# Kernel tuning notes

Measured on AMD Instinct MI355X. Metric: run time of the kernel, lower is better.

The kernel has to match this reference:

```python
import jax, jax.numpy as jnp
import numpy as np

L = 2048         # new tokens (prefill)
HID = 4096
NH = 32          # attention heads
NKV = 8          # kv heads
HD = HID // NH   # 128
MAX = 4096       # kv-cache capacity
EPS = 1e-5


def _rope_tables(L, HD):
    inv_freq = 1.0 / (10000.0 ** (np.arange(0, HD, 2, dtype=np.float32) / HD))
    ang = np.arange(L, dtype=np.float32)[:, None] * inv_freq[None, :]  # [L, HD/2]
    ang = np.concatenate([ang, ang], axis=-1)                          # HF duplicated layout
    return jnp.asarray(np.cos(ang)), jnp.asarray(np.sin(ang))


def setup_inputs() -> dict:
    key = jax.random.key(0)
    ks = jax.random.split(key, 6)
    cos, sin = _rope_tables(L, HD)
    s = 0.02
    return {
        "x": jax.random.normal(ks[0], (L, HID), jnp.float32),
        "cos": cos,
        "sin": sin,
        "position_ids": jnp.arange(L, dtype=jnp.int64),
        "seq_len": L,
        "k_cache": jnp.zeros((MAX, NKV, HD), jnp.float32),
        "v_cache": jnp.zeros((MAX, NKV, HD), jnp.float32),
        "ln_w": jnp.ones((HID,), jnp.float32),
        "Wq": jax.random.normal(ks[1], (NH * HD, HID), jnp.float32) * s,
        "Wk": jax.random.normal(ks[2], (NKV * HD, HID), jnp.float32) * s,
        "Wv": jax.random.normal(ks[3], (NKV * HD, HID), jnp.float32) * s,
        "Wo": jax.random.normal(ks[4], (HID, NH * HD), jnp.float32) * s,
    }


def _rms_norm(x, w, eps=EPS):
    xf = x.astype(jnp.float32)
    var = jnp.mean(xf * xf, axis=-1, keepdims=True)
    return (w * (xf * jax.lax.rsqrt(var + eps))).astype(x.dtype)


def _rotate_half(x):
    x1, x2 = jnp.split(x, 2, axis=-1)
    return jnp.concatenate([-x2, x1], axis=-1)


def reference(x, cos, sin, position_ids, seq_len, k_cache, v_cache, ln_w, Wq, Wk, Wv, Wo):
    Lq, hid = x.shape
    nkv, hd = k_cache.shape[1], k_cache.shape[2]
    nh = Wq.shape[0] // hd
    g = nh // nkv

    residual = x
    h = _rms_norm(x, ln_w)

    q = (h @ Wq.T).reshape(Lq, nh, hd)
    k = (h @ Wk.T).reshape(Lq, nkv, hd)
    v = (h @ Wv.T).reshape(Lq, nkv, hd)

    # RoPE, cos/sin broadcast over heads (unsqueeze_dim=1)
    c = cos[:, None, :]
    s = sin[:, None, :]
    q = q * c + _rotate_half(q) * s
    k = k * c + _rotate_half(k) * s

    # KV-cache scatter write
    k_cache = k_cache.at[position_ids].set(k)
    v_cache = v_cache.at[position_ids].set(v)

    # prefill path (num_new_tokens > 1): causal GQA SDPA over new keys only
    scale = 1.0 / jnp.sqrt(jnp.asarray(hd, jnp.float32))
    qg = q.reshape(Lq, nkv, g, hd)
    scores = jnp.einsum('qhgd,khd->hgqk', qg, k) * scale  # [nkv, g, Lq, Lq]
    idx = jnp.arange(Lq)
    causal = idx[None, :] <= idx[:, None]                  # [Lq, Lq]
    scores = jnp.where(causal[None, None], scores, -jnp.inf)
    p = jax.nn.softmax(scores, axis=-1)
    attn = jnp.einsum('hgqk,khd->qhgd', p, v).reshape(Lq, nh * hd)

    out = residual + attn @ Wo.T
    return out, k_cache, v_cache
```

## Files before the change

kernel.cpp:

```cpp
#include <hip/hip_runtime.h>
#include <hip/hip_bf16.h>
#include <cstdint>

#define L_SEQ 2048
#define HID   4096
#define NH    32
#define NKV   8
#define HD    128
#define MAXP  4096
#define QKVD  6144
#define K_OFF 4096
#define V_OFF 5120

using bf16_t = __hip_bfloat16;
typedef __bf16 bf16x8 __attribute__((ext_vector_type(8)));
typedef float  f32x4  __attribute__((ext_vector_type(4)));
typedef short  short4v __attribute__((ext_vector_type(4)));
typedef short  short8v __attribute__((ext_vector_type(8)));

__device__ __forceinline__ void async_copy16(void* lds, const void* g) {
  __builtin_amdgcn_global_load_lds(
      (__attribute__((address_space(1))) void*)g,
      (__attribute__((address_space(3))) void*)lds, 16, 0, 0);
}

__device__ __forceinline__ f32x4 MFMA16(bf16x8 a, bf16x8 b, f32x4 c) {
  return __builtin_amdgcn_mfma_f32_16x16x32_bf16(a, b, c, 0, 0, 0);
}

__global__ __launch_bounds__(256) void rmsnorm_kernel(
    const float* __restrict__ x, const float* __restrict__ w,
    bf16_t* __restrict__ h) {
  int row = blockIdx.x, t = threadIdx.x;
  const float4* xv = (const float4*)(x + (size_t)row * HID);
  float4 v[4];
  float ss = 0.f;
#pragma unroll
  for (int i = 0; i < 4; i++) {
    v[i] = xv[i * 256 + t];
    ss += v[i].x * v[i].x + v[i].y * v[i].y + v[i].z * v[i].z + v[i].w * v[i].w;
  }
#pragma unroll
  for (int off = 32; off >= 1; off >>= 1) ss += __shfl_xor(ss, off, 64);
  __shared__ float red[4];
  if ((t & 63) == 0) red[t >> 6] = ss;
  __syncthreads();
  float rr = rsqrtf((red[0] + red[1] + red[2] + red[3]) * (1.0f / HID) + 1e-5f);
  const float4* wv = (const float4*)w;
  bf16_t* hr = h + (size_t)row * HID;
#pragma unroll
  for (int i = 0; i < 4; i++) {
    float4 wl = wv[i * 256 + t];
    bf16_t tmp[4];
    tmp[0] = __float2bfloat16(v[i].x * rr * wl.x);
    tmp[1] = __float2bfloat16(v[i].y * rr * wl.y);
    tmp[2] = __float2bfloat16(v[i].z * rr * wl.z);
    tmp[3] = __float2bfloat16(v[i].w * rr * wl.w);
    *(short4v*)(hr + (size_t)(i * 256 + t) * 4) = *(short4v*)tmp;
  }
}

__global__ __launch_bounds__(256) void cvt_bf16_kernel(
    const float* __restrict__ src, bf16_t* __restrict__ dst) {
  size_t i = ((size_t)blockIdx.x * 256 + threadIdx.x) * 8;
  float4 a = *(const float4*)(src + i);
  float4 b = *(const float4*)(src + i + 4);
  bf16_t tmp[8] = {__float2bfloat16(a.x), __float2bfloat16(a.y),
                   __float2bfloat16(a.z), __float2bfloat16(a.w),
                   __float2bfloat16(b.x), __float2bfloat16(b.y),
                   __float2bfloat16(b.z), __float2bfloat16(b.w)};
  *(short8v*)(dst + i) = *(short8v*)tmp;
}

#define STR2_(x) #x
#define STR_(x) STR2_(x)

template <int OUT_MODE>
__global__ __launch_bounds__(512, 2) void gemm256_kernel(
    const bf16_t* __restrict__ A, const bf16_t* __restrict__ B,
    bf16_t* __restrict__ Cb, float* __restrict__ Cf,
    const float* __restrict__ resid, int N, int K) {
  __shared__ alignas(16) bf16_t As[2 * 2 * 8192];
  __shared__ alignas(16) bf16_t Bs[2 * 2 * 8192];

  const int t = threadIdx.x;
  const int l = t & 63;
  const int w = t >> 6;
  const int wm = w >> 2;
  const int wn = w & 3;
  const int wh = wn >> 1;
  const int wn1 = wn & 1;
  const int lane15 = l & 15, quad = l >> 4;
  const int l7 = l & 7;

  const bf16_t* Ag = A + (size_t)blockIdx.y * 256 * K;
  const bf16_t* Bg = B + (size_t)blockIdx.x * 256 * K;

  const int srow = t >> 3;
  const int sgran = (t & 7) ^ (srow & 7);
  const int wbase = w << 9;

  const bf16_t* pAg = Ag + (size_t)srow * K + sgran * 8;
  const bf16_t* pBg = Bg + (size_t)srow * K + sgran * 8;
  const size_t row64 = (size_t)64 * K;

#define STAGE(PL, UOFF, ldsh) do {                                            \
    const bf16_t* _g = (PL) + (UOFF);                                         \
    async_copy16((ldsh) + wbase, _g);                                         \
    async_copy16((ldsh) + wbase + 4096, _g + row64);                          \
  } while (0)

#define ASD(sl, h) (&As[(sl) * 16384 + (h) * 8192])
#define BSD(sl, h) (&Bs[(sl) * 16384 + (h) * 8192])

  typedef __attribute__((address_space(3))) char* lds_b;
  lds_b asb = (lds_b)As;
  lds_b bsb = (lds_b)Bs;
  const unsigned aoff0 = (unsigned)(wm * 16384 + lane15 * 128 + ((quad ^ l7) << 4));
  const unsigned boff0 = (unsigned)(wh * 16384 + (wn1 * 64 + lane15) * 128 + ((quad ^ l7) << 4));
  lds_b pa0s0 = asb + aoff0;
  lds_b pa1s0 = asb + (aoff0 ^ 64u);
  lds_b pa0s1 = pa0s0 + 32768;
  lds_b pa1s1 = pa1s0 + 32768;
  lds_b pb0s0 = bsb + boff0;
  lds_b pb1s0 = bsb + (boff0 ^ 64u);
  lds_b pb0s1 = pb0s0 + 32768;
  lds_b pb1s1 = pb1s0 + 32768;

#define DSR(dst, p, IMM) \
  asm volatile("ds_read_b128 %0, %1 offset:" STR_(IMM) : "=v"(dst) : "v"(p))

#define RA(dst, P0, P1, I0, I1, I2, I3) do {                                  \
    DSR(dst[0][0], P0, I0); DSR(dst[0][1], P1, I0);                           \
    DSR(dst[1][0], P0, I1); DSR(dst[1][1], P1, I1);                           \
    DSR(dst[2][0], P0, I2); DSR(dst[2][1], P1, I2);                           \
    DSR(dst[3][0], P0, I3); DSR(dst[3][1], P1, I3); } while (0)
#define RB(dst, P0, P1, I0, I1) do {                                          \
    DSR(dst[0][0], P0, I0); DSR(dst[0][1], P1, I0);                           \
    DSR(dst[1][0], P0, I1); DSR(dst[1][1], P1, I1); } while (0)

#define BAR() do { asm volatile("s_barrier");                                 \
    __builtin_amdgcn_sched_barrier(0); } while (0)
#define LGKM(NW) do { asm volatile("s_waitcnt lgkmcnt(" STR_(NW) ")");        \
    __builtin_amdgcn_sched_barrier(0); } while (0)
#define VMW(NW) asm volatile("s_waitcnt vmcnt(" STR_(NW) ")")

#define MMQ(IB, JB, AF, BF) do {                                              \
    __builtin_amdgcn_s_setprio(1);                                            \
    _Pragma("unroll") for (int i = 0; i < 4; i++)                             \
    _Pragma("unroll") for (int j = 0; j < 2; j++) {                           \
      acc[(IB)+i][(JB)+j] = MFMA16(AF[i][0], BF[j][0], acc[(IB)+i][(JB)+j]);  \
      acc[(IB)+i][(JB)+j] = MFMA16(AF[i][1], BF[j][1], acc[(IB)+i][(JB)+j]);  \
    }                                                                         \
    __builtin_amdgcn_s_setprio(0);                                            \
    __builtin_amdgcn_sched_barrier(0);                                        \
  } while (0)

  const size_t u128 = (size_t)128 * K;
  const int NTT = K >> 6;
  const int niter = NTT >> 1;

  f32x4 acc[8][4] = {};
  bf16x8 a[4][2], a2[4][2], blo[2][2], bhi[2][2];

  STAGE(pBg, 0,          BSD(0, 0));
  STAGE(pAg, 0,          ASD(0, 0));
  STAGE(pBg, u128,       BSD(0, 1));
  STAGE(pAg, u128,       ASD(0, 1));
  STAGE(pBg, 64,         BSD(1, 0));
  STAGE(pAg, 64,         ASD(1, 0));
  VMW(4);
  BAR();
  RA(a, pa0s0, pa1s0, 0, 2048, 4096, 6144);
  RB(blo, pb0s0, pb1s0, 0, 2048);

  for (int it = 0; it < niter; ++it) {
    const int tb = it * 2;
    const size_t kc1 = (size_t)((tb + 1) << 6);
    const size_t kc2 = (size_t)(((tb + 2 < NTT) ? tb + 2 : NTT - 1) << 6);
    const size_t kc3 = (size_t)(((tb + 3 < NTT) ? tb + 3 : NTT - 1) << 6);
    STAGE(pBg, u128 + kc1, BSD(1, 1));
    BAR();
    RB(bhi, pb0s0, pb1s0, 4096, 6144);
    LGKM(4);
    MMQ(0, 0, a, blo);
    BAR();
    STAGE(pAg, u128 + kc1, ASD(1, 1));
    BAR();
    RA(a2, pa0s0, pa1s0, 8192, 10240, 12288, 14336);
    LGKM(8);
    MMQ(0, 2, a, bhi);
    BAR();
    STAGE(pBg, kc2, BSD(0, 0));
    BAR();
    LGKM(0);
    MMQ(4, 0, a2, blo);
    BAR();
    STAGE(pAg, kc2, ASD(0, 0));
    VMW(4);
    BAR();
    RA(a, pa0s1, pa1s1, 0, 2048, 4096, 6144);
    RB(blo, pb0s1, pb1s1, 0, 2048);
    LGKM(12);
    MMQ(4, 2, a2, bhi);
    BAR();
    STAGE(pBg, u128 + kc2, BSD(0, 1));
    BAR();
    RB(bhi, pb0s1, pb1s1, 4096, 6144);
    LGKM(4);
    MMQ(0, 0, a, blo);
    BAR();
    STAGE(pAg, u128 + kc2, ASD(0, 1));
    BAR();
    RA(a2, pa0s1, pa1s1, 8192, 10240, 12288, 14336);
    LGKM(8);
    MMQ(0, 2, a, bhi);
    BAR();
    STAGE(pBg, kc3, BSD(1, 0));
    BAR();
    LGKM(0);
    MMQ(4, 0, a2, blo);
    BAR();
    STAGE(pAg, kc3, ASD(1, 0));
    VMW(4);
    BAR();
    if (it + 1 < niter) {
      RA(a, pa0s0, pa1s0, 0, 2048, 4096, 6144);
      RB(blo, pb0s0, pb1s0, 0, 2048);
    }
    LGKM(12);
    MMQ(4, 2, a2, bhi);
    BAR();
  }
  VMW(0);

  const int row0 = blockIdx.y * 256 + wm * 128 + quad * 4;
  const int col0 = blockIdx.x * 256 + wn * 64 + lane15;
#pragma unroll
  for (int i = 0; i < 8; i++)
#pragma unroll
    for (int j = 0; j < 4; j++)
#pragma unroll
      for (int r = 0; r < 4; r++) {
        size_t idx = (size_t)(row0 + i * 16 + r) * N + col0 + j * 16;
        if (OUT_MODE == 0)
          Cb[idx] = __float2bfloat16(acc[i][j][r]);
        else
          Cf[idx] = acc[i][j][r] + resid[idx];
      }
#undef STAGE
#undef ASD
#undef BSD
#undef DSR
#undef RA
#undef RB
#undef BAR
#undef LGKM
#undef VMW
#undef MMQ
}

__global__ __launch_bounds__(256) void rope_kernel(
    bf16_t* __restrict__ qkv,
    const float* __restrict__ cosT, const float* __restrict__ sinT,
    float* __restrict__ kc_out) {
  int idx = blockIdx.x * 256 + threadIdx.x;
  int d = idx & 63;
  int rest = idx >> 6;
  int hh = rest % (NH + NKV);
  int pos = rest / (NH + NKV);
  float c = cosT[pos * HD + d];
  float s = sinT[pos * HD + d];
  bf16_t* b = (hh < NH)
      ? qkv + (size_t)pos * QKVD + hh * HD
      : qkv + (size_t)pos * QKVD + K_OFF + (hh - NH) * HD;
  float x1 = __bfloat162float(b[d]);
  float x2 = __bfloat162float(b[d + 64]);
  float o1 = x1 * c - x2 * s;
  float o2 = x2 * c + x1 * s;
  b[d] = __float2bfloat16(o1);
  b[d + 64] = __float2bfloat16(o2);
  if (hh >= NH) {
    float* kc = kc_out + (size_t)pos * (NKV * HD) + (hh - NH) * HD;
    kc[d] = o1;
    kc[d + 64] = o2;
  }
}

__global__ __launch_bounds__(256) void vtrans_kernel(
    const bf16_t* __restrict__ qkv, float* __restrict__ vc_out,
    bf16_t* __restrict__ vT) {
  __shared__ alignas(16) short Ts[64 * 64];
  int kvh = blockIdx.x, pb = blockIdx.y, db = blockIdx.z;
  int t = threadIdx.x;
  int r = t & 63;
  int c4 = t >> 6;
  const short* src = (const short*)(qkv + (size_t)(pb * 64 + r) * QKVD +
                                    V_OFF + kvh * HD + db * 64 + c4 * 16);
  short8v v0 = *(const short8v*)src;
  short8v v1 = *(const short8v*)(src + 8);
  float* vo = vc_out + (size_t)(pb * 64 + r) * (NKV * HD) + kvh * HD + db * 64 + c4 * 16;
  float tmpf[16];
#pragma unroll
  for (int j = 0; j < 8; j++) {
    tmpf[j]     = __uint_as_float(((unsigned)(unsigned short)v0[j]) << 16);
    tmpf[j + 8] = __uint_as_float(((unsigned)(unsigned short)v1[j]) << 16);
  }
#pragma unroll
  for (int j = 0; j < 4; j++)
    ((float4*)vo)[j] = make_float4(tmpf[j * 4], tmpf[j * 4 + 1],
                                   tmpf[j * 4 + 2], tmpf[j * 4 + 3]);
  int cs = c4 ^ (r & 3);
  *(short8v*)&Ts[r * 64 + cs * 16] = v0;
  *(short8v*)&Ts[r * 64 + cs * 16 + 8] = v1;
  __syncthreads();
  int dr = t & 63;
  int pc = t >> 6;
  short vals[16];
#pragma unroll
  for (int j = 0; j < 16; j++) {
    int pos = pc * 16 + j;
    int cc = (dr >> 4) ^ (pos & 3);
    vals[j] = Ts[pos * 64 + cc * 16 + (dr & 15)];
  }
  short* dst = (short*)(vT + ((size_t)kvh * HD + db * 64 + dr) * L_SEQ + pb * 64 + pc * 16);
  *(short8v*)dst = *(short8v*)&vals[0];
  *(short8v*)(dst + 8) = *(short8v*)&vals[8];
}

__global__ __launch_bounds__(256) void cache_tail_kernel(
    const float* __restrict__ kc_in, const float* __restrict__ vc_in,
    float* __restrict__ kc_out, float* __restrict__ vc_out) {
  size_t base = (size_t)L_SEQ * NKV * HD;
  size_t i = base + ((size_t)blockIdx.x * 256 + threadIdx.x) * 4;
  *(float4*)(kc_out + i) = *(const float4*)(kc_in + i);
  *(float4*)(vc_out + i) = *(const float4*)(vc_in + i);
}

__global__ __launch_bounds__(256) void attn_kernel(
    const bf16_t* __restrict__ qkv, const bf16_t* __restrict__ vT,
    bf16_t* __restrict__ attn) {
  int h = blockIdx.x;
  int qblk = blockIdx.y;
  int kvh = h >> 2;
  int t = threadIdx.x, w = t >> 6, l = t & 63;
  int lane15 = l & 15, quad = l >> 4;

  __shared__ alignas(16) bf16_t Ks[16 * 512];
  __shared__ alignas(16) bf16_t Vs[16 * 512];
  __shared__ alignas(16) bf16_t Ps[4][32 * 68];

  bf16x8 aq[2][4];
#pragma unroll
  for (int i = 0; i < 2; i++)
#pragma unroll
    for (int kk = 0; kk < 4; kk++)
      aq[i][kk] = *(const bf16x8*)(qkv +
          (size_t)(qblk * 128 + w * 32 + i * 16 + lane15) * QKVD +
          h * HD + kk * 32 + quad * 8);

  f32x4 o[2][8] = {};
  float lsum[2][4] = {};
  const float scale = 0.08838834764831845f;
  int rowmax_w = qblk * 128 + w * 32 + 31;
  int nk = 2 * qblk + 2;

  for (int kblk = 0; kblk < nk; kblk++) {
    __syncthreads();
#pragma unroll
    for (int kk = 0; kk < 4; kk++)
      async_copy16(&Ks[(w * 4 + kk) * 512],
                   qkv + (size_t)(kblk * 64 + w * 16 + lane15) * QKVD +
                       K_OFF + kvh * HD + kk * 32 + quad * 8);
#pragma unroll
    for (int j = 0; j < 4; j++) {
      int tt = w * 2 + (j >> 1), kt2 = j & 1;
      async_copy16(&Vs[(tt * 2 + kt2) * 512],
                   vT + ((size_t)kvh * HD + tt * 16 + lane15) * L_SEQ +
                       kblk * 64 + kt2 * 32 + quad * 8);
    }
    __syncthreads();

    if (kblk * 64 <= rowmax_w) {
      f32x4 sacc[2][4] = {};
#pragma unroll
      for (int n = 0; n < 4; n++)
#pragma unroll
        for (int kk = 0; kk < 4; kk++) {
          bf16x8 b = *(const bf16x8*)&Ks[(n * 4 + kk) * 512 + l * 8];
          sacc[0][n] = __builtin_amdgcn_mfma_f32_16x16x32_bf16(aq[0][kk], b, sacc[0][n], 0, 0, 0);
          sacc[1][n] = __builtin_amdgcn_mfma_f32_16x16x32_bf16(aq[1][kk], b, sacc[1][n], 0, 0, 0);
        }
      bool maskblk = (kblk >= 2 * qblk);
#pragma unroll
      for (int i = 0; i < 2; i++)
#pragma unroll
        for (int n = 0; n < 4; n++) {
          int col = kblk * 64 + n * 16 + lane15;
#pragma unroll
          for (int r = 0; r < 4; r++) {
            float p = __expf(sacc[i][n][r] * scale);
            if (maskblk && col > (qblk * 128 + w * 32 + i * 16 + quad * 4 + r)) p = 0.f;
            lsum[i][r] += p;
            Ps[w][(i * 16 + quad * 4 + r) * 68 + n * 16 + lane15] = __float2bfloat16(p);
          }
        }
#pragma unroll
      for (int i = 0; i < 2; i++)
#pragma unroll
        for (int kt2 = 0; kt2 < 2; kt2++) {
          bf16x8 ap = *(const bf16x8*)&Ps[w][(i * 16 + lane15) * 68 + kt2 * 32 + quad * 8];
#pragma unroll
          for (int tt = 0; tt < 8; tt++) {
            bf16x8 b = *(const bf16x8*)&Vs[(tt * 2 + kt2) * 512 + l * 8];
            o[i][tt] = __builtin_amdgcn_mfma_f32_16x16x32_bf16(ap, b, o[i][tt], 0, 0, 0);
          }
        }
    }
  }

  float inv[2][4];
#pragma unroll
  for (int i = 0; i < 2; i++)
#pragma unroll
    for (int r = 0; r < 4; r++) {
      float s = lsum[i][r];
#pragma unroll
      for (int off = 1; off < 16; off <<= 1) s += __shfl_xor(s, off, 64);
      inv[i][r] = 1.f / s;
    }
  int qrow0 = qblk * 128 + w * 32;
#pragma unroll
  for (int i = 0; i < 2; i++)
#pragma unroll
    for (int tt = 0; tt < 8; tt++) {
      int col = h * HD + tt * 16 + lane15;
#pragma unroll
      for (int r = 0; r < 4; r++)
        attn[(size_t)(qrow0 + i * 16 + quad * 4 + r) * HID + col] =
            __float2bfloat16(o[i][tt][r] * inv[i][r]);
    }
}

extern "C" void kernel_launch(void* const* d_in, const int* in_sizes, int n_in,
                              void* d_out, int out_size, void* d_ws, size_t ws_size,
                              hipStream_t stream) {
  const float* x    = (const float*)d_in[0];
  const float* cosT = (const float*)d_in[1];
  const float* sinT = (const float*)d_in[2];
  const float* kc_in = (const float*)d_in[5];
  const float* vc_in = (const float*)d_in[6];
  const float* ln_w  = (const float*)d_in[7];
  const float* Wq = (const float*)d_in[8];
  const float* Wk = (const float*)d_in[9];
  const float* Wv = (const float*)d_in[10];
  const float* Wo = (const float*)d_in[11];

  float* out    = (float*)d_out;
  float* kc_out = out + (size_t)L_SEQ * HID;
  float* vc_out = kc_out + (size_t)MAXP * NKV * HD;

  char* ws = (char*)d_ws;
  bf16_t* h_bf    = (bf16_t*)(ws + 0);
  bf16_t* attn_bf = (bf16_t*)(ws + 0);
  bf16_t* Wqkv_bf = (bf16_t*)(ws + 16777216);
  bf16_t* Wo_bf   = (bf16_t*)(ws + 16777216);
  bf16_t* qkv_bf  = (bf16_t*)(ws + 67108864);
  bf16_t* vT_bf   = (bf16_t*)(ws + 92274688);

  rmsnorm_kernel<<<L_SEQ, 256, 0, stream>>>(x, ln_w, h_bf);
  cvt_bf16_kernel<<<(HID * HID) / (8 * 256), 256, 0, stream>>>(Wq, Wqkv_bf);
  cvt_bf16_kernel<<<(NKV * HD * HID) / (8 * 256), 256, 0, stream>>>(
      Wk, Wqkv_bf + (size_t)K_OFF * HID);
  cvt_bf16_kernel<<<(NKV * HD * HID) / (8 * 256), 256, 0, stream>>>(
      Wv, Wqkv_bf + (size_t)V_OFF * HID);

  gemm256_kernel<0><<<dim3(QKVD / 256, L_SEQ / 256), 512, 0, stream>>>(
      h_bf, Wqkv_bf, qkv_bf, nullptr, nullptr, QKVD, HID);

  rope_kernel<<<(L_SEQ * (NH + NKV) * 64) / 256, 256, 0, stream>>>(
      qkv_bf, cosT, sinT, kc_out);
  vtrans_kernel<<<dim3(NKV, L_SEQ / 64, HD / 64), 256, 0, stream>>>(
      qkv_bf, vc_out, vT_bf);
  cache_tail_kernel<<<((MAXP - L_SEQ) * NKV * HD) / (4 * 256), 256, 0, stream>>>(
      kc_in, vc_in, kc_out, vc_out);

  cvt_bf16_kernel<<<(HID * HID) / (8 * 256), 256, 0, stream>>>(Wo, Wo_bf);

  attn_kernel<<<dim3(NH, L_SEQ / 128), 256, 0, stream>>>(qkv_bf, vT_bf, attn_bf);

  gemm256_kernel<1><<<dim3(HID / 256, L_SEQ / 256), 512, 0, stream>>>(
      attn_bf, Wo_bf, nullptr, out, x, HID, HID);
}
```

Before: 575.6 us.

## Pair causal q-blocks per workgroup and double-buffer K/V tiles in attention

Each attention workgroup now handles two query blocks, qblk and 15-qblk, so causal work is balanced across a grid half as large. K/V tiles are double-buffered in LDS: the next tile's async copy is issued before computing on the current one, with explicit vmcnt waits and raw barriers replacing the full __syncthreads pair. s_setprio is raised around the MFMA sections. The cost is doubled LDS use, which may limit occupancy, and fewer workgroups in flight.

```diff
diff --git a/kernel.cpp b/kernel.cpp
--- a/kernel.cpp
+++ b/kernel.cpp
@@ -341,105 +341,124 @@
     const bf16_t* __restrict__ qkv, const bf16_t* __restrict__ vT,
     bf16_t* __restrict__ attn) {
   int h = blockIdx.x;
-  int qblk = blockIdx.y;
   int kvh = h >> 2;
   int t = threadIdx.x, w = t >> 6, l = t & 63;
   int lane15 = l & 15, quad = l >> 4;
 
-  __shared__ alignas(16) bf16_t Ks[16 * 512];
-  __shared__ alignas(16) bf16_t Vs[16 * 512];
+  __shared__ alignas(16) bf16_t Ks[2][16 * 512];
+  __shared__ alignas(16) bf16_t Vs[2][16 * 512];
   __shared__ alignas(16) bf16_t Ps[4][32 * 68];
 
-  bf16x8 aq[2][4];
-#pragma unroll
-  for (int i = 0; i < 2; i++)
-#pragma unroll
-    for (int kk = 0; kk < 4; kk++)
-      aq[i][kk] = *(const bf16x8*)(qkv +
-          (size_t)(qblk * 128 + w * 32 + i * 16 + lane15) * QKVD +
-          h * HD + kk * 32 + quad * 8);
-
-  f32x4 o[2][8] = {};
-  float lsum[2][4] = {};
   const float scale = 0.08838834764831845f;
-  int rowmax_w = qblk * 128 + w * 32 + 31;
-  int nk = 2 * qblk + 2;
-
-  for (int kblk = 0; kblk < nk; kblk++) {
-    __syncthreads();
-#pragma unroll
-    for (int kk = 0; kk < 4; kk++)
-      async_copy16(&Ks[(w * 4 + kk) * 512],
-                   qkv + (size_t)(kblk * 64 + w * 16 + lane15) * QKVD +
-                       K_OFF + kvh * HD + kk * 32 + quad * 8);
-#pragma unroll
-    for (int j = 0; j < 4; j++) {
-      int tt = w * 2 + (j >> 1), kt2 = j & 1;
-      async_copy16(&Vs[(tt * 2 + kt2) * 512],
-                   vT + ((size_t)kvh * HD + tt * 16 + lane15) * L_SEQ +
-                       kblk * 64 + kt2 * 32 + quad * 8);
+
+#define STAGEATTN(KB, BUF) do {                                               \
+    _Pragma("unroll") for (int kk_ = 0; kk_ < 4; kk_++)                       \
+      async_copy16(&Ks[BUF][(w * 4 + kk_) * 512],                             \
+                   qkv + (size_t)((KB) * 64 + w * 16 + lane15) * QKVD +       \
+                       K_OFF + kvh * HD + kk_ * 32 + quad * 8);               \
+    _Pragma("unroll") for (int j_ = 0; j_ < 4; j_++) {                        \
+      int tt_ = w * 2 + (j_ >> 1), kt_ = j_ & 1;                              \
+      async_copy16(&Vs[BUF][(tt_ * 2 + kt_) * 512],                           \
+                   vT + ((size_t)kvh * HD + tt_ * 16 + lane15) * L_SEQ +      \
+                       (KB) * 64 + kt_ * 32 + quad * 8);                      \
+    }                                                                         \
+  } while (0)
+
+  for (int sel = 0; sel < 2; ++sel) {
+    const int qblk = sel ? 15 - (int)blockIdx.y : (int)blockIdx.y;
+
+    bf16x8 aq[2][4];
+#pragma unroll
+    for (int i = 0; i < 2; i++)
+#pragma unroll
+      for (int kk = 0; kk < 4; kk++)
+        aq[i][kk] = *(const bf16x8*)(qkv +
+            (size_t)(qblk * 128 + w * 32 + i * 16 + lane15) * QKVD +
+            h * HD + kk * 32 + quad * 8);
+
+    f32x4 o[2][8] = {};
+    float lsum[2][4] = {};
+    int rowmax_w = qblk * 128 + w * 32 + 31;
+    int nk = 2 * qblk + 2;
+
+    STAGEATTN(0, 0);
+    for (int kblk = 0; kblk < nk; kblk++) {
+      const int cur = kblk & 1;
+      if (kblk + 1 < nk) {
+        STAGEATTN(kblk + 1, cur ^ 1);
+        asm volatile("s_waitcnt vmcnt(8)");
+      } else {
+        asm volatile("s_waitcnt vmcnt(0)");
+      }
+      __builtin_amdgcn_s_barrier();
+      __builtin_amdgcn_sched_barrier(0);
+
+      if (kblk * 64 <= rowmax_w) {
+        f32x4 sacc[2][4] = {};
+        __builtin_amdgcn_s_setprio(1);
+#pragma unroll
+        for (int n = 0; n < 4; n++)
+#pragma unroll
+          for (int kk = 0; kk < 4; kk++) {
+            bf16x8 b = *(const bf16x8*)&Ks[cur][(n * 4 + kk) * 512 + l * 8];
+            sacc[0][n] = MFMA16(aq[0][kk], b, sacc[0][n]);
+            sacc[1][n] = MFMA16(aq[1][kk], b, sacc[1][n]);
+          }
+        __builtin_amdgcn_s_setprio(0);
+        bool maskblk = (kblk >= 2 * qblk);
+#pragma unroll
+        for (int i = 0; i < 2; i++)
+#pragma unroll
+          for (int n = 0; n < 4; n++) {
+            int col = kblk * 64 + n * 16 + lane15;
+#pragma unroll
+            for (int r = 0; r < 4; r++) {
+              float p = __expf(sacc[i][n][r] * scale);
+              if (maskblk && col > (qblk * 128 + w * 32 + i * 16 + quad * 4 + r)) p = 0.f;
+              lsum[i][r] += p;
+              Ps[w][(i * 16 + quad * 4 + r) * 68 + n * 16 + lane15] = __float2bfloat16(p);
+            }
+          }
+        __builtin_amdgcn_s_setprio(1);
+#pragma unroll
+        for (int i = 0; i < 2; i++)
+#pragma unroll
+          for (int kt2 = 0; kt2 < 2; kt2++) {
+            bf16x8 ap = *(const bf16x8*)&Ps[w][(i * 16 + lane15) * 68 + kt2 * 32 + quad * 8];
+#pragma unroll
+            for (int tt = 0; tt < 8; tt++) {
+              bf16x8 b = *(const bf16x8*)&Vs[cur][(tt * 2 + kt2) * 512 + l * 8];
+              o[i][tt] = MFMA16(ap, b, o[i][tt]);
+            }
+          }
+        __builtin_amdgcn_s_setprio(0);
+      }
+      __builtin_amdgcn_s_barrier();
     }
-    __syncthreads();
-
-    if (kblk * 64 <= rowmax_w) {
-      f32x4 sacc[2][4] = {};
-#pragma unroll
-      for (int n = 0; n < 4; n++)
-#pragma unroll
-        for (int kk = 0; kk < 4; kk++) {
-          bf16x8 b = *(const bf16x8*)&Ks[(n * 4 + kk) * 512 + l * 8];
-          sacc[0][n] = __builtin_amdgcn_mfma_f32_16x16x32_bf16(aq[0][kk], b, sacc[0][n], 0, 0, 0);
-          sacc[1][n] = __builtin_amdgcn_mfma_f32_16x16x32_bf16(aq[1][kk], b, sacc[1][n], 0, 0, 0);
-        }
-      bool maskblk = (kblk >= 2 * qblk);
-#pragma unroll
-      for (int i = 0; i < 2; i++)
-#pragma unroll
-        for (int n = 0; n < 4; n++) {
-          int col = kblk * 64 + n * 16 + lane15;
-#pragma unroll
-          for (int r = 0; r < 4; r++) {
-            float p = __expf(sacc[i][n][r] * scale);
-            if (maskblk && col > (qblk * 128 + w * 32 + i * 16 + quad * 4 + r)) p = 0.f;
-            lsum[i][r] += p;
-            Ps[w][(i * 16 + quad * 4 + r) * 68 + n * 16 + lane15] = __float2bfloat16(p);
-          }
-        }
-#pragma unroll
-      for (int i = 0; i < 2; i++)
-#pragma unroll
-        for (int kt2 = 0; kt2 < 2; kt2++) {
-          bf16x8 ap = *(const bf16x8*)&Ps[w][(i * 16 + lane15) * 68 + kt2 * 32 + quad * 8];
-#pragma unroll
-          for (int tt = 0; tt < 8; tt++) {
-            bf16x8 b = *(const bf16x8*)&Vs[(tt * 2 + kt2) * 512 + l * 8];
-            o[i][tt] = __builtin_amdgcn_mfma_f32_16x16x32_bf16(ap, b, o[i][tt], 0, 0, 0);
-          }
-        }
-    }
-  }
-
-  float inv[2][4];
-#pragma unroll
-  for (int i = 0; i < 2; i++)
-#pragma unroll
-    for (int r = 0; r < 4; r++) {
-      float s = lsum[i][r];
-#pragma unroll
-      for (int off = 1; off < 16; off <<= 1) s += __shfl_xor(s, off, 64);
-      inv[i][r] = 1.f / s;
-    }
-  int qrow0 = qblk * 128 + w * 32;
-#pragma unroll
-  for (int i = 0; i < 2; i++)
-#pragma unroll
-    for (int tt = 0; tt < 8; tt++) {
-      int col = h * HD + tt * 16 + lane15;
-#pragma unroll
-      for (int r = 0; r < 4; r++)
-        attn[(size_t)(qrow0 + i * 16 + quad * 4 + r) * HID + col] =
-            __float2bfloat16(o[i][tt][r] * inv[i][r]);
-    }
+
+    float inv[2][4];
+#pragma unroll
+    for (int i = 0; i < 2; i++)
+#pragma unroll
+      for (int r = 0; r < 4; r++) {
+        float s = lsum[i][r];
+#pragma unroll
+        for (int off = 1; off < 16; off <<= 1) s += __shfl_xor(s, off, 64);
+        inv[i][r] = 1.f / s;
+      }
+    int qrow0 = qblk * 128 + w * 32;
+#pragma unroll
+    for (int i = 0; i < 2; i++)
+#pragma unroll
+      for (int tt = 0; tt < 8; tt++) {
+        int col = h * HD + tt * 16 + lane15;
+#pragma unroll
+        for (int r = 0; r < 4; r++)
+          attn[(size_t)(qrow0 + i * 16 + quad * 4 + r) * HID + col] =
+              __float2bfloat16(o[i][tt][r] * inv[i][r]);
+      }
+  }
+#undef STAGEATTN
 }
 
 extern "C" void kernel_launch(void* const* d_in, const int* in_sizes, int n_in,
@@ -487,7 +506,7 @@
 
   cvt_bf16_kernel<<<(HID * HID) / (8 * 256), 256, 0, stream>>>(Wo, Wo_bf);
 
-  attn_kernel<<<dim3(NH, L_SEQ / 128), 256, 0, stream>>>(qkv_bf, vT_bf, attn_bf);
+  attn_kernel<<<dim3(NH, 8), 256, 0, stream>>>(qkv_bf, vT_bf, attn_bf);
 
   gemm256_kernel<1><<<dim3(HID / 256, L_SEQ / 256), 512, 0, stream>>>(
       attn_bf, Wo_bf, nullptr, out, x, HID, HID);
```

Result: no change. 579.0 us (+0.6%).
